# Performance work log

Hardware: AMD Instinct MI355X
Metric: run time of the kernel (lower is better)

Reference implementation:

```python
import jax, jax.numpy as jnp
import numpy as np

B, DIN, D, C, M, NF = 64, 150528, 512, 100, 64, 256
EPS = 1e-6


def setup_inputs() -> dict:
    key = jax.random.key(0)
    ks = jax.random.split(key, 6)
    image = jax.random.normal(ks[0], (B, DIN), jnp.float32) * 0.02
    W_enc = jax.random.normal(ks[1], (DIN, D), jnp.float32) * 0.01
    text = jax.random.normal(ks[2], (C, D), jnp.float32)
    text_features = text / jnp.linalg.norm(text, axis=-1, keepdims=True)
    keys = jax.random.normal(ks[3], (C, M, D), jnp.float32)
    keys_all = keys / jnp.linalg.norm(keys, axis=-1, keepdims=True)
    indices = jax.random.randint(ks[4], (C, NF), 0, D, dtype=jnp.int32)
    return {
        "image": image,
        "W_enc": W_enc,
        "text_features": text_features,
        "keys_all": keys_all,
        "logit_scale": jnp.float32(np.log(100.0)),
        "indices": indices,
        "alpha": jnp.float32(1.0),
        "beta": jnp.float32(5.5),
        "gamma": jnp.float32(0.1),
    }


def reference(image, W_enc, text_features, keys_all, logit_scale, indices, alpha, beta, gamma):
    # image encoder (dense GEMM stand-in for clip_model.visual) + L2 normalize
    f = image @ W_enc                                    # [B, D]
    f = f / jnp.linalg.norm(f, axis=-1, keepdims=True)
    clip_logits = jnp.exp(logit_scale) * (f @ text_features.T)   # [B, C]

    # per-class feature-dim gathers (vectorized over classes)
    keys_sel = jax.vmap(lambda k, idx: k[:, idx])(keys_all, indices)      # [C, M, NF]
    text_sel = jax.vmap(lambda idx: text_features[:, idx])(indices)       # [C, C, NF]  (text_sel[c, j, f])
    img_sel = f[:, indices]                                               # [B, C, NF]

    # cache similarities: per-class [B, M] matmul, scaled by number of keys
    sims = jnp.einsum('bcf,cmf->bcm', img_sel, keys_sel) / M              # [B, C, M]

    # key logits and softmax over classes
    key_logits = jax.nn.softmax(jnp.einsum('cmf,cjf->cmj', keys_sel, text_sel), axis=-1)  # [C, M, C]

    # KL(one_hot(c) || key_logits) in log2; only the j==c term is nonzero
    p_cc = key_logits[jnp.arange(C)[:, None], jnp.arange(M)[None, :], jnp.arange(C)[:, None]]  # [C, M]
    KL = jnp.log2((1.0 + EPS) / (p_cc + EPS))                             # [C, M]
    w = jnp.exp(KL * gamma)                                               # soft_values nonzero entries

    # block-diagonal soft_values => cache_logits[b, c] = sum_m sims[b, c, m] * w[c, m]
    cache = jnp.einsum('bcm,cm->bc', sims, w)                             # [B, C]
    cache_logits = jnp.exp(-(beta - beta * cache))
    return alpha * cache_logits + clip_logits
```

## Files before the change

### kernel.cpp

```cpp
#include <hip/hip_runtime.h>

#define DIN 150528
#define DD 512
#define NC 100
#define NM 64
#define NFEAT 256
#define EPSF 1e-6f
#define KSTEPS (DIN / 32)

typedef float f32x4 __attribute__((ext_vector_type(4)));
typedef __bf16 bf16x8 __attribute__((ext_vector_type(8)));
typedef unsigned short u16x8 __attribute__((ext_vector_type(8)));

static __device__ __forceinline__ unsigned short f2bf(float x) {
  unsigned int u = __builtin_bit_cast(unsigned int, x);
  u += 0x7FFFu + ((u >> 16) & 1u);
  return (unsigned short)(u >> 16);
}
static __device__ __forceinline__ float bf2f(unsigned short h) {
  return __builtin_bit_cast(float, ((unsigned int)h) << 16);
}

__global__ __launch_bounds__(256, 1) void gemm_f(
    const float* __restrict__ image, const float* __restrict__ W,
    float* __restrict__ f_buf) {
  const int tid = threadIdx.x;
  const int wv = tid >> 6;
  const int lane = tid & 63;
  const int q = lane >> 4;
  const int r16 = lane & 15;
  const int nb = wv * 128;

  f32x4 acc[4][8];
#pragma unroll
  for (int mt = 0; mt < 4; ++mt)
#pragma unroll
    for (int nt = 0; nt < 8; ++nt)
#pragma unroll
      for (int r = 0; r < 4; ++r) acc[mt][nt][r] = 0.0f;

  const int b = blockIdx.x;
  const int s0 = (b * KSTEPS) >> 8;
  const int s1 = ((b + 1) * KSTEPS) >> 8;

  for (int s = s0; s < s1; ++s) {
    const int k0 = s * 32;
    f32x4 alo[4], ahi[4];
#pragma unroll
    for (int mt = 0; mt < 4; ++mt) {
      const float* ap = image + (size_t)(mt * 16 + r16) * DIN + (k0 + q * 8);
      alo[mt] = *(const f32x4*)ap;
      ahi[mt] = *(const f32x4*)(ap + 4);
    }
    float wr[8][8];
#pragma unroll
    for (int nt = 0; nt < 8; ++nt) {
      const float* wp = W + (size_t)(k0 + q * 8) * DD + (nb + nt * 16 + r16);
#pragma unroll
      for (int j = 0; j < 8; ++j) wr[nt][j] = wp[(size_t)j * DD];
    }
    bf16x8 av[4];
#pragma unroll
    for (int mt = 0; mt < 4; ++mt) {
      u16x8 u;
      u[0] = f2bf(alo[mt][0]); u[1] = f2bf(alo[mt][1]);
      u[2] = f2bf(alo[mt][2]); u[3] = f2bf(alo[mt][3]);
      u[4] = f2bf(ahi[mt][0]); u[5] = f2bf(ahi[mt][1]);
      u[6] = f2bf(ahi[mt][2]); u[7] = f2bf(ahi[mt][3]);
      av[mt] = __builtin_bit_cast(bf16x8, u);
    }
    bf16x8 bv[8];
#pragma unroll
    for (int nt = 0; nt < 8; ++nt) {
      u16x8 u;
#pragma unroll
      for (int j = 0; j < 8; ++j) u[j] = f2bf(wr[nt][j]);
      bv[nt] = __builtin_bit_cast(bf16x8, u);
    }
#pragma unroll
    for (int mt = 0; mt < 4; ++mt)
#pragma unroll
      for (int nt = 0; nt < 8; ++nt)
        acc[mt][nt] = __builtin_amdgcn_mfma_f32_16x16x32_bf16(
            av[mt], bv[nt], acc[mt][nt], 0, 0, 0);
  }

#pragma unroll
  for (int mt = 0; mt < 4; ++mt)
#pragma unroll
    for (int nt = 0; nt < 8; ++nt) {
      const int n = nb + nt * 16 + r16;
#pragma unroll
      for (int r = 0; r < 4; ++r) {
        const int m = mt * 16 + q * 4 + r;
        atomicAdd(f_buf + m * DD + n, acc[mt][nt][r]);
      }
    }
}

__global__ void norm_f(const float* __restrict__ f, float* __restrict__ fn) {
  const int b = blockIdx.x;
  const int t = threadIdx.x;
  float s = 0.0f;
#pragma unroll
  for (int i = 0; i < 8; ++i) {
    float v = f[b * DD + t + i * 64];
    s += v * v;
  }
#pragma unroll
  for (int o = 32; o; o >>= 1) s += __shfl_xor(s, o);
  const float inv = 1.0f / sqrtf(s);
#pragma unroll
  for (int i = 0; i < 8; ++i)
    fn[b * DD + t + i * 64] = f[b * DD + t + i * 64] * inv;
}

__global__ __launch_bounds__(256) void wk_kernel(
    const float* __restrict__ text, const float* __restrict__ keys,
    const int* __restrict__ indices, const float* __restrict__ pgamma,
    float* __restrict__ kw_buf) {
  const int c = blockIdx.x;
  const int t = threadIdx.x;
  const int wv = t >> 6, lane = t & 63;
  const int q = lane >> 4, r16 = lane & 15;

  __shared__ __align__(16) unsigned short A_lds[64 * 264];
  __shared__ __align__(16) unsigned short B_lds[112 * 136];
  __shared__ __align__(16) int idx_s[256];

  idx_s[t] = indices[c * 256 + t];
  __syncthreads();

  {
    const int j = t;
    const float* kp = keys + (size_t)c * 64 * 512 + idx_s[j];
#pragma unroll 8
    for (int m = 0; m < 64; ++m) A_lds[m * 264 + j] = f2bf(kp[(size_t)m * 512]);
  }

  f32x4 acc[7];
#pragma unroll
  for (int nt = 0; nt < 7; ++nt)
#pragma unroll
    for (int r = 0; r < 4; ++r) acc[nt][r] = 0.0f;
  const int mt = wv;

  for (int kh = 0; kh < 2; ++kh) {
    __syncthreads();
    {
      const int kk = t & 127;
      const float* tp = text + idx_s[kh * 128 + kk];
      for (int n = (t >> 7); n < 112; n += 2)
        B_lds[n * 136 + kk] =
            (n < NC) ? f2bf(tp[(size_t)n * 512]) : (unsigned short)0;
    }
    __syncthreads();
#pragma unroll
    for (int ks = 0; ks < 4; ++ks) {
      bf16x8 afr = *(const bf16x8*)(A_lds + (mt * 16 + r16) * 264 + kh * 128 +
                                    ks * 32 + q * 8);
#pragma unroll
      for (int nt = 0; nt < 7; ++nt) {
        bf16x8 bfr =
            *(const bf16x8*)(B_lds + (nt * 16 + r16) * 136 + ks * 32 + q * 8);
        acc[nt] = __builtin_amdgcn_mfma_f32_16x16x32_bf16(afr, bfr, acc[nt],
                                                          0, 0, 0);
      }
    }
  }
  __syncthreads();

  float* C_lds = reinterpret_cast<float*>(B_lds);
#pragma unroll
  for (int nt = 0; nt < 7; ++nt) {
    const int j2 = nt * 16 + r16;
#pragma unroll
    for (int r = 0; r < 4; ++r) {
      const int m = mt * 16 + q * 4 + r;
      C_lds[m * 113 + j2] = acc[nt][r];
    }
  }
  __syncthreads();

  float* w_lds = reinterpret_cast<float*>(idx_s);
  if (t < 64) {
    const int m = t;
    float mx = -1e30f;
    for (int j2 = 0; j2 < NC; ++j2) mx = fmaxf(mx, C_lds[m * 113 + j2]);
    float sum = 0.0f;
    for (int j2 = 0; j2 < NC; ++j2) sum += expf(C_lds[m * 113 + j2] - mx);
    const float p = expf(C_lds[m * 113 + c] - mx) / sum;
    const float KL = log2f((1.0f + EPSF) / (p + EPSF));
    w_lds[m] = expf(KL * (*pgamma));
  }
  __syncthreads();
  {
    const int j = t;
    float kwv = 0.0f;
#pragma unroll 8
    for (int m = 0; m < 64; ++m) kwv += w_lds[m] * bf2f(A_lds[m * 264 + j]);
    kw_buf[c * 256 + j] = kwv;
  }
}

__global__ __launch_bounds__(256) void final_kernel(
    const float* __restrict__ fn, const float* __restrict__ text,
    const int* __restrict__ indices, const float* __restrict__ kw_buf,
    const float* __restrict__ pls, const float* __restrict__ palpha,
    const float* __restrict__ pbeta, float* __restrict__ out) {
  const int c = blockIdx.x;
  const int t = threadIdx.x;
  const int wv = t >> 6, lane = t & 63;
  __shared__ float redc[4], redl[4];

  const int myidx = indices[c * 256 + t];
  const float mykw = kw_buf[c * 256 + t];
  const float tc0 = text[c * 512 + t];
  const float tc1 = text[c * 512 + 256 + t];
  const float ls = expf(*pls);
  const float alpha = *palpha, beta = *pbeta;

  for (int b = 0; b < 64; ++b) {
    const float* fr = fn + b * 512;
    float cp = fr[myidx] * mykw;
    float lp = fr[t] * tc0 + fr[t + 256] * tc1;
#pragma unroll
    for (int o = 32; o; o >>= 1) {
      cp += __shfl_xor(cp, o);
      lp += __shfl_xor(lp, o);
    }
    if (lane == 0) { redc[wv] = cp; redl[wv] = lp; }
    __syncthreads();
    if (t == 0) {
      const float cache = (redc[0] + redc[1] + redc[2] + redc[3]) * (1.0f / 64.0f);
      const float clip = (redl[0] + redl[1] + redl[2] + redl[3]) * ls;
      out[b * 100 + c] = alpha * expf(beta * cache - beta) + clip;
    }
    __syncthreads();
  }
}

extern "C" void kernel_launch(void* const* d_in, const int* in_sizes, int n_in,
                              void* d_out, int out_size, void* d_ws,
                              size_t ws_size, hipStream_t stream) {
  const float* image = (const float*)d_in[0];
  const float* W = (const float*)d_in[1];
  const float* text = (const float*)d_in[2];
  const float* keys = (const float*)d_in[3];
  const float* pls = (const float*)d_in[4];
  const int* idx = (const int*)d_in[5];
  const float* palpha = (const float*)d_in[6];
  const float* pbeta = (const float*)d_in[7];
  const float* pgamma = (const float*)d_in[8];
  float* out = (float*)d_out;

  char* ws = (char*)d_ws;
  float* f_buf = (float*)(ws);
  float* fn = (float*)(ws + 131072);
  float* kw = (float*)(ws + 262144);

  hipMemsetAsync(f_buf, 0, 64 * 512 * sizeof(float), stream);
  gemm_f<<<256, 256, 0, stream>>>(image, W, f_buf);
  norm_f<<<64, 64, 0, stream>>>(f_buf, fn);
  wk_kernel<<<NC, 256, 0, stream>>>(text, keys, idx, pgamma, kw);
  final_kernel<<<NC, 256, 0, stream>>>(fn, text, idx, kw, pls, palpha, pbeta,
                                       out);
}
```

Baseline: 555.6 us.

## Replace atomic split-K reduction with partial buffers and reduce kernel; barrier-free final

The split-K GEMM now writes each block's 64x512 partial result to its own slice of a 32 MB workspace instead of issuing float atomicAdds into a shared buffer, and a new reduce kernel sums the 256 partials. The memset is dropped. The final kernel now gives each wavefront its own batch rows, which removes the LDS reduction and the per-row __syncthreads. The aim is to avoid atomic contention and barrier overhead, at the cost of about 64 MB of extra global traffic and one more launch.

```diff
diff --git a/kernel.cpp b/kernel.cpp
--- a/kernel.cpp
+++ b/kernel.cpp
@@ -23,7 +23,7 @@
 
 __global__ __launch_bounds__(256, 1) void gemm_f(
     const float* __restrict__ image, const float* __restrict__ W,
-    float* __restrict__ f_buf) {
+    float* __restrict__ f_part) {
   const int tid = threadIdx.x;
   const int wv = tid >> 6;
   const int lane = tid & 63;
@@ -85,6 +85,7 @@
             av[mt], bv[nt], acc[mt][nt], 0, 0, 0);
   }
 
+  float* outp = f_part + (size_t)b * (NM * DD);
 #pragma unroll
   for (int mt = 0; mt < 4; ++mt)
 #pragma unroll
@@ -93,9 +94,20 @@
 #pragma unroll
       for (int r = 0; r < 4; ++r) {
         const int m = mt * 16 + q * 4 + r;
-        atomicAdd(f_buf + m * DD + n, acc[mt][nt][r]);
+        outp[m * DD + n] = acc[mt][nt][r];
       }
     }
+}
+
+__global__ __launch_bounds__(128) void reduce_f(
+    const float* __restrict__ f_part, float* __restrict__ f) {
+  const int m = blockIdx.x >> 2;
+  const int n = (blockIdx.x & 3) * 128 + threadIdx.x;
+  const float* p = f_part + (size_t)m * DD + n;
+  float s = 0.0f;
+#pragma unroll 16
+  for (int sdx = 0; sdx < 256; ++sdx) s += p[(size_t)sdx * (NM * DD)];
+  f[m * DD + n] = s;
 }
 
 __global__ void norm_f(const float* __restrict__ f, float* __restrict__ fn) {
@@ -209,34 +221,36 @@
     const float* __restrict__ pls, const float* __restrict__ palpha,
     const float* __restrict__ pbeta, float* __restrict__ out) {
   const int c = blockIdx.x;
-  const int t = threadIdx.x;
-  const int wv = t >> 6, lane = t & 63;
-  __shared__ float redc[4], redl[4];
-
-  const int myidx = indices[c * 256 + t];
-  const float mykw = kw_buf[c * 256 + t];
-  const float tc0 = text[c * 512 + t];
-  const float tc1 = text[c * 512 + 256 + t];
+  const int wv = threadIdx.x >> 6, lane = threadIdx.x & 63;
+
+  int idx4[4];
+  float kw4[4];
+#pragma unroll
+  for (int i = 0; i < 4; ++i) {
+    idx4[i] = indices[c * 256 + i * 64 + lane];
+    kw4[i] = kw_buf[c * 256 + i * 64 + lane];
+  }
+  float tc[8];
+#pragma unroll
+  for (int i = 0; i < 8; ++i) tc[i] = text[c * 512 + i * 64 + lane];
   const float ls = expf(*pls);
   const float alpha = *palpha, beta = *pbeta;
 
-  for (int b = 0; b < 64; ++b) {
-    const float* fr = fn + b * 512;
-    float cp = fr[myidx] * mykw;
-    float lp = fr[t] * tc0 + fr[t + 256] * tc1;
+  for (int b = wv; b < 64; b += 4) {
+    const float* fr = fn + b * DD;
+    float cp = 0.0f, lp = 0.0f;
+#pragma unroll
+    for (int i = 0; i < 4; ++i) cp += fr[idx4[i]] * kw4[i];
+#pragma unroll
+    for (int i = 0; i < 8; ++i) lp += fr[i * 64 + lane] * tc[i];
 #pragma unroll
     for (int o = 32; o; o >>= 1) {
       cp += __shfl_xor(cp, o);
       lp += __shfl_xor(lp, o);
     }
-    if (lane == 0) { redc[wv] = cp; redl[wv] = lp; }
-    __syncthreads();
-    if (t == 0) {
-      const float cache = (redc[0] + redc[1] + redc[2] + redc[3]) * (1.0f / 64.0f);
-      const float clip = (redl[0] + redl[1] + redl[2] + redl[3]) * ls;
-      out[b * 100 + c] = alpha * expf(beta * cache - beta) + clip;
-    }
-    __syncthreads();
+    if (lane == 0)
+      out[b * NC + c] =
+          alpha * expf(beta * (cp * (1.0f / 64.0f)) - beta) + ls * lp;
   }
 }
 
@@ -255,12 +269,13 @@
   float* out = (float*)d_out;
 
   char* ws = (char*)d_ws;
-  float* f_buf = (float*)(ws);
-  float* fn = (float*)(ws + 131072);
-  float* kw = (float*)(ws + 262144);
-
-  hipMemsetAsync(f_buf, 0, 64 * 512 * sizeof(float), stream);
-  gemm_f<<<256, 256, 0, stream>>>(image, W, f_buf);
+  float* f_part = (float*)(ws);
+  float* f_buf = (float*)(ws + 33554432);
+  float* fn = (float*)(ws + 33554432 + 131072);
+  float* kw = (float*)(ws + 33554432 + 262144);
+
+  gemm_f<<<256, 256, 0, stream>>>(image, W, f_part);
+  reduce_f<<<256, 128, 0, stream>>>(f_part, f_buf);
   norm_f<<<64, 64, 0, stream>>>(f_buf, fn);
   wk_kernel<<<NC, 256, 0, stream>>>(text, keys, idx, pgamma, kw);
   final_kernel<<<NC, 256, 0, stream>>>(fn, text, idx, kw, pls, palpha, pbeta,
```

New measurement: 510.3 us. 8.2% less time.
